# Performance work log

Hardware: AMD Instinct MI355X
Metric: run time of the kernel (lower is better)

The kernel has to match this reference:

```python
import jax, jax.numpy as jnp
import numpy as np

V, H, E = 32000, 1024, 1024
B, S = 64, 128

def setup_inputs() -> dict:
    key = jax.random.key(0)
    ks = jax.random.split(key, 14)
    sc = 0.02
    return {
        "input_batch": jax.random.randint(ks[0], (B, 1), 0, V),
        "prev_h": jax.random.normal(ks[1], (1, B, H), jnp.float32),
        "prev_c": jax.random.normal(ks[2], (1, B, H), jnp.float32),
        "encoder_outputs": jax.random.normal(ks[3], (B, S, H), jnp.float32),
        "lengths": jnp.ones((B,), jnp.int64 if jax.config.read('jax_enable_x64') else jnp.int32),
        "emb": jax.random.normal(ks[4], (V, E), jnp.float32) * sc,
        "attn_w": jax.random.normal(ks[5], (2 * H,), jnp.float32) * sc,
        "attn_b": jax.random.normal(ks[6], (1,), jnp.float32) * sc,
        "W_ih": jax.random.normal(ks[7], (4 * H, E + H), jnp.float32) * sc,
        "W_hh": jax.random.normal(ks[8], (4 * H, H), jnp.float32) * sc,
        "b_ih": jax.random.normal(ks[9], (4 * H,), jnp.float32) * sc,
        "b_hh": jax.random.normal(ks[10], (4 * H,), jnp.float32) * sc,
        "W_out": jax.random.normal(ks[11], (V, H), jnp.float32) * sc,
        "b_out": jax.random.normal(ks[12], (V,), jnp.float32) * sc,
    }

def reference(input_batch, prev_h, prev_c, encoder_outputs, lengths,
              emb, attn_w, attn_b, W_ih, W_hh, b_ih, b_hh, W_out, b_out):
    h0 = prev_h[0]            # [B, H]
    c0 = prev_c[0]            # [B, H]
    x_emb = emb[input_batch[:, 0]]  # [B, E]

    # attention: score[b,s] = concat(h0[b], enc[b,s]) @ attn_w + attn_b
    # (vectorized form of the original per-element Python loop)
    h_part = h0 @ attn_w[:H]                                   # [B]
    e_part = jnp.einsum('bsh,h->bs', encoder_outputs, attn_w[H:])  # [B, S]
    scores = e_part + h_part[:, None] + attn_b[0]
    attn_weights = jax.nn.softmax(scores, axis=-1)             # [B, S]
    context = jnp.einsum('bs,bsh->bh', attn_weights, encoder_outputs)  # [B, H]

    # single-step LSTM cell (torch gate order: i, f, g, o)
    x = jnp.concatenate([x_emb, context], axis=-1)             # [B, E+H]
    gates = x @ W_ih.T + h0 @ W_hh.T + b_ih + b_hh             # [B, 4H]
    i_g, f_g, g_g, o_g = jnp.split(gates, 4, axis=-1)
    c1 = jax.nn.sigmoid(f_g) * c0 + jax.nn.sigmoid(i_g) * jnp.tanh(g_g)
    h1 = jax.nn.sigmoid(o_g) * jnp.tanh(c1)

    # zero-out rows with length == 0
    zmask = (lengths == 0)[:, None]                            # [B, 1]
    h1 = jnp.where(zmask, 0.0, h1)
    c1 = jnp.where(zmask, 0.0, c1)

    logits = h1 @ W_out.T + b_out                              # [B, V]
    logprobs = jax.nn.log_softmax(logits, axis=-1)
    return (logprobs, h1[None], c1[None], attn_weights)
```

## Files before the change

kernel.cpp:

```cpp
#include <hip/hip_runtime.h>
#include <math.h>

constexpr int V = 32000, H = 1024, E = 1024, B = 64, S = 128;
constexpr int KX = 2048;

constexpr long long OUT_H1   = (long long)B * V;
constexpr long long OUT_C1   = OUT_H1 + (long long)B * H;
constexpr long long OUT_ATTN = OUT_C1 + (long long)B * H;

constexpr long long WS_SCORES = 0;
constexpr long long WS_XCAT   = WS_SCORES + (long long)B * S;
constexpr long long WS_PART   = WS_XCAT + (long long)B * KX;
constexpr long long WS_CTXP   = WS_PART + 6LL * B * 4096;
constexpr long long WS_PM     = WS_CTXP + 4LL * B * H;
constexpr long long WS_PL     = WS_PM + 64 * 512;
constexpr long long WS_LC     = WS_PL + 64 * 512;

typedef __attribute__((ext_vector_type(8))) short short8;
typedef __attribute__((ext_vector_type(4))) float f32x4;

__device__ __forceinline__ unsigned short f2bf(float f) {
  unsigned u = __float_as_uint(f);
  u += 0x7FFF + ((u >> 16) & 1);
  return (unsigned short)(u >> 16);
}

__device__ __forceinline__ short8 pack8(float4 a, float4 b) {
  short8 s;
  s[0] = (short)f2bf(a.x); s[1] = (short)f2bf(a.y);
  s[2] = (short)f2bf(a.z); s[3] = (short)f2bf(a.w);
  s[4] = (short)f2bf(b.x); s[5] = (short)f2bf(b.y);
  s[6] = (short)f2bf(b.z); s[7] = (short)f2bf(b.w);
  return s;
}

__device__ __forceinline__ void gemm_body(
    const float* __restrict__ W, int ldw,
    const float* __restrict__ X, int ldx,
    int g0, int k0, int KC,
    float* __restrict__ dst, int ldo, const float* __restrict__ bias,
    float* __restrict__ pm, float* __restrict__ pl) {
  __shared__ __align__(16) unsigned short Wl[64 * 64];
  __shared__ __align__(16) unsigned short Xl[64 * 64];
  __shared__ float pmx[4][64];
  __shared__ float psm[4][64];
  int t = threadIdx.x;
  int lane = t & 63, wid = t >> 6;
  int n = lane & 15, quad = lane >> 4;
  int r0 = t >> 3,          c0 = t & 7;
  int r1 = (t + 256) >> 3,  c1 = (t + 256) & 7;
  int ws0 = r0 * 64 + (c0 ^ (r0 & 7)) * 8;
  int ws1 = r1 * 64 + (c1 ^ (r1 & 7)) * 8;
  f32x4 acc[4] = {{0.f,0.f,0.f,0.f},{0.f,0.f,0.f,0.f},
                  {0.f,0.f,0.f,0.f},{0.f,0.f,0.f,0.f}};
  const float* wp0 = W + (long long)(g0 + r0) * ldw + k0 + c0 * 8;
  const float* wp1 = W + (long long)(g0 + r1) * ldw + k0 + c1 * 8;
  const float* xp0 = X + (long long)r0 * ldx + k0 + c0 * 8;
  const float* xp1 = X + (long long)r1 * ldx + k0 + c1 * 8;
  float4 wa = ((const float4*)wp0)[0], wb = ((const float4*)wp0)[1];
  float4 wc = ((const float4*)wp1)[0], wd = ((const float4*)wp1)[1];
  float4 xa = ((const float4*)xp0)[0], xb = ((const float4*)xp0)[1];
  float4 xc = ((const float4*)xp1)[0], xd = ((const float4*)xp1)[1];

  for (int kt = 0; kt < KC; kt += 64) {
    __syncthreads();
    *(short8*)&Wl[ws0] = pack8(wa, wb);
    *(short8*)&Wl[ws1] = pack8(wc, wd);
    *(short8*)&Xl[ws0] = pack8(xa, xb);
    *(short8*)&Xl[ws1] = pack8(xc, xd);
    __syncthreads();
    if (kt + 64 < KC) {
      int o = kt + 64;
      wa = *(const float4*)(wp0 + o); wb = *(const float4*)(wp0 + o + 4);
      wc = *(const float4*)(wp1 + o); wd = *(const float4*)(wp1 + o + 4);
      xa = *(const float4*)(xp0 + o); xb = *(const float4*)(xp0 + o + 4);
      xc = *(const float4*)(xp1 + o); xd = *(const float4*)(xp1 + o + 4);
    }
#pragma unroll
    for (int kc = 0; kc < 2; ++kc) {
      short8 af = *(const short8*)&Wl[(wid * 16 + n) * 64 +
                                      (((kc * 4 + quad) ^ (n & 7)) * 8)];
#pragma unroll
      for (int nt = 0; nt < 4; ++nt) {
        short8 bf = *(const short8*)&Xl[(nt * 16 + n) * 64 +
                                        (((kc * 4 + quad) ^ (n & 7)) * 8)];
        acc[nt] = __builtin_amdgcn_mfma_f32_16x16x32_bf16(af, bf, acc[nt], 0, 0, 0);
      }
    }
  }
  int gl = wid * 16 + quad * 4;
  float bs[4] = {0.f, 0.f, 0.f, 0.f};
  if (bias) {
#pragma unroll
    for (int r = 0; r < 4; ++r) bs[r] = bias[g0 + gl + r];
  }
  float v[4][4];
#pragma unroll
  for (int nt = 0; nt < 4; ++nt) {
    int b = nt * 16 + n;
#pragma unroll
    for (int r = 0; r < 4; ++r) {
      v[nt][r] = acc[nt][r] + bs[r];
      dst[(long long)b * ldo + g0 + gl + r] = v[nt][r];
    }
  }
  if (pm) {
    float tmax[4];
#pragma unroll
    for (int nt = 0; nt < 4; ++nt) {
      tmax[nt] = fmaxf(fmaxf(v[nt][0], v[nt][1]), fmaxf(v[nt][2], v[nt][3]));
      tmax[nt] = fmaxf(tmax[nt], __shfl_xor(tmax[nt], 16, 64));
      tmax[nt] = fmaxf(tmax[nt], __shfl_xor(tmax[nt], 32, 64));
    }
    if (lane < 16) {
#pragma unroll
      for (int nt = 0; nt < 4; ++nt) pmx[wid][nt * 16 + lane] = tmax[nt];
    }
    __syncthreads();
    float bmax[4], tsum[4];
#pragma unroll
    for (int nt = 0; nt < 4; ++nt) {
      bmax[nt] = fmaxf(fmaxf(pmx[0][nt * 16 + n], pmx[1][nt * 16 + n]),
                       fmaxf(pmx[2][nt * 16 + n], pmx[3][nt * 16 + n]));
      tsum[nt] = __expf(v[nt][0] - bmax[nt]) + __expf(v[nt][1] - bmax[nt]) +
                 __expf(v[nt][2] - bmax[nt]) + __expf(v[nt][3] - bmax[nt]);
      tsum[nt] += __shfl_xor(tsum[nt], 16, 64);
      tsum[nt] += __shfl_xor(tsum[nt], 32, 64);
    }
    if (lane < 16) {
#pragma unroll
      for (int nt = 0; nt < 4; ++nt) psm[wid][nt * 16 + lane] = tsum[nt];
    }
    __syncthreads();
    if (t < 64) {
      float M = fmaxf(fmaxf(pmx[0][t], pmx[1][t]), fmaxf(pmx[2][t], pmx[3][t]));
      float L = psm[0][t] + psm[1][t] + psm[2][t] + psm[3][t];
      pm[t * 512 + blockIdx.x] = M;
      pl[t * 512 + blockIdx.x] = L;
    }
  }
}

__global__ __launch_bounds__(256) void k_gates_mfma(
    const float* __restrict__ W_ih, const float* __restrict__ xcat,
    const float* __restrict__ W_hh, const float* __restrict__ h0,
    float* __restrict__ part) {
  int y = blockIdx.y;
  if (y < 4)
    gemm_body(W_ih, KX, xcat, KX, blockIdx.x * 64, y * 512, 512,
              part + (long long)y * B * 4096, 4096, nullptr, nullptr, nullptr);
  else
    gemm_body(W_hh, H, h0, H, blockIdx.x * 64, (y - 4) * 512, 512,
              part + (long long)y * B * 4096, 4096, nullptr, nullptr, nullptr);
}

__global__ __launch_bounds__(256) void k_logits_mfma(
    const float* __restrict__ W_out, const float* __restrict__ h1,
    float* __restrict__ logits, const float* __restrict__ b_out,
    float* __restrict__ pm, float* __restrict__ pl) {
  gemm_body(W_out, H, h1, H, blockIdx.x * 64, 0, H, logits, V, b_out, pm, pl);
}

__global__ __launch_bounds__(256) void k_scores(
    const float* __restrict__ enc, const float* __restrict__ attn_w,
    float* __restrict__ scores) {
  int w = (blockIdx.x * 256 + threadIdx.x) >> 6;
  int lane = threadIdx.x & 63;
  const float4* e4 = (const float4*)(enc + (long long)w * H);
  const float4* w4 = (const float4*)(attn_w + H);
  float acc = 0.f;
#pragma unroll
  for (int i = 0; i < 4; ++i) {
    float4 a = e4[lane + 64 * i];
    float4 b = w4[lane + 64 * i];
    acc += a.x * b.x + a.y * b.y + a.z * b.z + a.w * b.w;
  }
#pragma unroll
  for (int m = 32; m; m >>= 1) acc += __shfl_xor(acc, m, 64);
  if (lane == 0) scores[w] = acc;
}

__global__ __launch_bounds__(128) void k_softmax(
    const float* __restrict__ scores, const float* __restrict__ h0,
    const float* __restrict__ attn_w, const float* __restrict__ attn_b,
    float* __restrict__ attn_out) {
  __shared__ float red[128];
  int b = blockIdx.x, t = threadIdx.x;
  float p = 0.f;
#pragma unroll
  for (int j = 0; j < 8; ++j) {
    int k = t + 128 * j;
    p += h0[b * H + k] * attn_w[k];
  }
  red[t] = p; __syncthreads();
  for (int off = 64; off > 0; off >>= 1) {
    if (t < off) red[t] += red[t + off];
    __syncthreads();
  }
  float hp = red[0]; __syncthreads();
  float sc = scores[b * S + t] + hp + attn_b[0];
  red[t] = sc; __syncthreads();
  for (int off = 64; off > 0; off >>= 1) {
    if (t < off) red[t] = fmaxf(red[t], red[t + off]);
    __syncthreads();
  }
  float m = red[0]; __syncthreads();
  float e = expf(sc - m);
  red[t] = e; __syncthreads();
  for (int off = 64; off > 0; off >>= 1) {
    if (t < off) red[t] += red[t + off];
    __syncthreads();
  }
  attn_out[b * S + t] = e / red[0];
}

__global__ __launch_bounds__(256) void k_ctx(
    const float* __restrict__ enc, const float* __restrict__ aw_in,
    float* __restrict__ ctxp) {
  __shared__ float aw[32];
  int b = blockIdx.x, sq = blockIdx.y, t = threadIdx.x;
  if (t < 32) aw[t] = aw_in[b * S + sq * 32 + t];
  __syncthreads();
  const float4* e4 = (const float4*)enc;
  float4 acc = {0.f, 0.f, 0.f, 0.f};
  for (int s = 0; s < 32; ++s) {
    float a = aw[s];
    float4 v = e4[(long long)(b * S + sq * 32 + s) * (H / 4) + t];
    acc.x += a * v.x; acc.y += a * v.y; acc.z += a * v.z; acc.w += a * v.w;
  }
  ((float4*)ctxp)[(long long)(sq * B + b) * (H / 4) + t] = acc;
}

__global__ __launch_bounds__(256) void k_xcat(
    const float* __restrict__ ctxp, const float* __restrict__ emb,
    const int* __restrict__ idx, float* __restrict__ xcat) {
  int ft = blockIdx.x * 256 + threadIdx.x;
  int b = ft >> 8, hq = ft & 255;
  const float4* c4 = (const float4*)ctxp;
  float4 ctx = c4[(0 * B + b) * 256 + hq];
#pragma unroll
  for (int sq = 1; sq < 4; ++sq) {
    float4 v = c4[(sq * B + b) * 256 + hq];
    ctx.x += v.x; ctx.y += v.y; ctx.z += v.z; ctx.w += v.w;
  }
  float4* x4 = (float4*)xcat;
  x4[b * 512 + hq]       = ((const float4*)emb)[(long long)idx[b] * 256 + hq];
  x4[b * 512 + 256 + hq] = ctx;
}

__global__ __launch_bounds__(256) void k_lstm(
    const float* __restrict__ part, const float* __restrict__ b_ih,
    const float* __restrict__ b_hh, const float* __restrict__ c0,
    const int* __restrict__ lengths,
    float* __restrict__ h1, float* __restrict__ c1) {
  int ft = blockIdx.x * 256 + threadIdx.x;
  int b = ft >> 10, h = ft & 1023;
  float gs[4] = {0.f, 0.f, 0.f, 0.f};
  for (int ks = 0; ks < 6; ++ks) {
    const float* p = part + (long long)(ks * B + b) * 4096;
#pragma unroll
    for (int q = 0; q < 4; ++q) gs[q] += p[q * H + h];
  }
#pragma unroll
  for (int q = 0; q < 4; ++q) gs[q] += b_ih[q * H + h] + b_hh[q * H + h];
  float ig = 1.f / (1.f + expf(-gs[0]));
  float fg = 1.f / (1.f + expf(-gs[1]));
  float gg = tanhf(gs[2]);
  float og = 1.f / (1.f + expf(-gs[3]));
  float c = fg * c0[ft] + ig * gg;
  float hh = og * tanhf(c);
  if (lengths[b] == 0) { c = 0.f; hh = 0.f; }
  h1[ft] = hh; c1[ft] = c;
}

__global__ __launch_bounds__(256) void k_lsm_comb(
    const float* __restrict__ pm, const float* __restrict__ pl,
    float* __restrict__ lc) {
  __shared__ float red[256];
  int b = blockIdx.x, t = threadIdx.x;
  float v0 = pm[b * 512 + t];
  float v1 = (t + 256 < 500) ? pm[b * 512 + t + 256] : -INFINITY;
  red[t] = fmaxf(v0, v1); __syncthreads();
  for (int off = 128; off; off >>= 1) {
    if (t < off) red[t] = fmaxf(red[t], red[t + off]);
    __syncthreads();
  }
  float M = red[0]; __syncthreads();
  float s = pl[b * 512 + t] * __expf(v0 - M);
  if (t + 256 < 500) s += pl[b * 512 + t + 256] * __expf(v1 - M);
  red[t] = s; __syncthreads();
  for (int off = 128; off; off >>= 1) {
    if (t < off) red[t] += red[t + off];
    __syncthreads();
  }
  if (t == 0) lc[b] = M + logf(red[0]);
}

__global__ __launch_bounds__(256) void k_lsm_fin(
    float* __restrict__ logits, const float* __restrict__ lc) {
  int fi = blockIdx.x * 256 + threadIdx.x;
  float4* p = (float4*)logits;
  float4 x = p[fi];
  float c = lc[fi / 8000];
  x.x -= c; x.y -= c; x.z -= c; x.w -= c;
  p[fi] = x;
}

extern "C" void kernel_launch(void* const* d_in, const int* in_sizes, int n_in,
                              void* d_out, int out_size, void* d_ws, size_t ws_size,
                              hipStream_t stream) {
  const int*   input_batch = (const int*)d_in[0];
  const float* prev_h = (const float*)d_in[1];
  const float* prev_c = (const float*)d_in[2];
  const float* enc    = (const float*)d_in[3];
  const int*   lengths= (const int*)d_in[4];
  const float* emb    = (const float*)d_in[5];
  const float* attn_w = (const float*)d_in[6];
  const float* attn_b = (const float*)d_in[7];
  const float* W_ih   = (const float*)d_in[8];
  const float* W_hh   = (const float*)d_in[9];
  const float* b_ih   = (const float*)d_in[10];
  const float* b_hh   = (const float*)d_in[11];
  const float* W_out  = (const float*)d_in[12];
  const float* b_out  = (const float*)d_in[13];

  float* out = (float*)d_out;
  float* ws  = (float*)d_ws;

  float* scores = ws + WS_SCORES;
  float* xcat   = ws + WS_XCAT;
  float* part   = ws + WS_PART;
  float* ctxp   = ws + WS_CTXP;
  float* pm     = ws + WS_PM;
  float* pl     = ws + WS_PL;
  float* lc     = ws + WS_LC;

  float* logits = out;
  float* h1     = out + OUT_H1;
  float* c1     = out + OUT_C1;
  float* attn   = out + OUT_ATTN;

  k_scores <<<dim3(B * S / 4), 256, 0, stream>>>(enc, attn_w, scores);
  k_softmax<<<dim3(B),         128, 0, stream>>>(scores, prev_h, attn_w, attn_b, attn);
  k_ctx    <<<dim3(B, 4),      256, 0, stream>>>(enc, attn, ctxp);
  k_xcat   <<<dim3(B * H / 1024), 256, 0, stream>>>(ctxp, emb, input_batch, xcat);

  k_gates_mfma<<<dim3(64, 6), 256, 0, stream>>>(W_ih, xcat, W_hh, prev_h, part);
  k_lstm   <<<dim3(B * H / 256), 256, 0, stream>>>(part, b_ih, b_hh, prev_c,
                                                   lengths, h1, c1);

  k_logits_mfma<<<dim3(V / 64), 256, 0, stream>>>(W_out, h1, logits, b_out, pm, pl);

  k_lsm_comb<<<dim3(B), 256, 0, stream>>>(pm, pl, lc);
  k_lsm_fin <<<dim3(B * V / 4 / 256), 256, 0, stream>>>(logits, lc);
}
```

Before: 354.2 us.

## Fuse attention stages into one kernel and logits+log-softmax into cooperative kernel

The scores, softmax, context and xcat kernels are merged into a single per-batch attention kernel, so the scores and context partials no longer round-trip through global memory. The logits GEMM, the log-softmax combine and the finalize pass are merged into one cooperative kernel that separates the phases with grid-wide syncs. This removes several kernel launches and intermediate buffers. In exchange the attention stage runs on only 64 blocks, which may underuse the GPU. The cooperative launch also needs all 500 blocks co-resident, and grid.sync has its own cost.

```diff
diff --git a/kernel.cpp b/kernel.cpp
--- a/kernel.cpp
+++ b/kernel.cpp
@@ -1,5 +1,8 @@
 #include <hip/hip_runtime.h>
+#include <hip/hip_cooperative_groups.h>
 #include <math.h>
+
+namespace cg = cooperative_groups;
 
 constexpr int V = 32000, H = 1024, E = 1024, B = 64, S = 128;
 constexpr int KX = 2048;
@@ -154,98 +157,77 @@
               part + (long long)y * B * 4096, 4096, nullptr, nullptr, nullptr);
 }
 
-__global__ __launch_bounds__(256) void k_logits_mfma(
-    const float* __restrict__ W_out, const float* __restrict__ h1,
-    float* __restrict__ logits, const float* __restrict__ b_out,
-    float* __restrict__ pm, float* __restrict__ pl) {
-  gemm_body(W_out, H, h1, H, blockIdx.x * 64, 0, H, logits, V, b_out, pm, pl);
-}
-
-__global__ __launch_bounds__(256) void k_scores(
-    const float* __restrict__ enc, const float* __restrict__ attn_w,
-    float* __restrict__ scores) {
-  int w = (blockIdx.x * 256 + threadIdx.x) >> 6;
-  int lane = threadIdx.x & 63;
-  const float4* e4 = (const float4*)(enc + (long long)w * H);
-  const float4* w4 = (const float4*)(attn_w + H);
-  float acc = 0.f;
-#pragma unroll
-  for (int i = 0; i < 4; ++i) {
-    float4 a = e4[lane + 64 * i];
-    float4 b = w4[lane + 64 * i];
-    acc += a.x * b.x + a.y * b.y + a.z * b.z + a.w * b.w;
-  }
-#pragma unroll
-  for (int m = 32; m; m >>= 1) acc += __shfl_xor(acc, m, 64);
-  if (lane == 0) scores[w] = acc;
-}
-
-__global__ __launch_bounds__(128) void k_softmax(
-    const float* __restrict__ scores, const float* __restrict__ h0,
+__global__ __launch_bounds__(256) void k_attn(
+    const float* __restrict__ enc, const float* __restrict__ h0,
     const float* __restrict__ attn_w, const float* __restrict__ attn_b,
-    float* __restrict__ attn_out) {
-  __shared__ float red[128];
+    const float* __restrict__ emb, const int* __restrict__ idx,
+    float* __restrict__ attn_out, float* __restrict__ xcat) {
+  __shared__ float red[256];
+  __shared__ float aw[S];
   int b = blockIdx.x, t = threadIdx.x;
-  float p = 0.f;
-#pragma unroll
-  for (int j = 0; j < 8; ++j) {
-    int k = t + 128 * j;
-    p += h0[b * H + k] * attn_w[k];
-  }
-  red[t] = p; __syncthreads();
-  for (int off = 64; off > 0; off >>= 1) {
+  int lane = t & 63, wv = t >> 6;
+  const float4* h4  = (const float4*)(h0 + (long long)b * H);
+  const float4* w4l = (const float4*)attn_w;
+  float4 hv = h4[t], wvv = w4l[t];
+  float p = hv.x * wvv.x + hv.y * wvv.y + hv.z * wvv.z + hv.w * wvv.w;
+#pragma unroll
+  for (int m = 32; m; m >>= 1) p += __shfl_xor(p, m, 64);
+  if (lane == 0) red[wv] = p;
+  __syncthreads();
+  float hp = red[0] + red[1] + red[2] + red[3] + attn_b[0];
+  const float4* w4h = (const float4*)(attn_w + H);
+  float4 wreg[4];
+#pragma unroll
+  for (int j = 0; j < 4; ++j) wreg[j] = w4h[lane + 64 * j];
+  __syncthreads();
+  for (int i = 0; i < 32; ++i) {
+    int s = wv * 32 + i;
+    const float4* e4 = (const float4*)(enc + (long long)(b * S + s) * H);
+    float a = 0.f;
+#pragma unroll
+    for (int j = 0; j < 4; ++j) {
+      float4 e = e4[lane + 64 * j];
+      a += e.x * wreg[j].x + e.y * wreg[j].y + e.z * wreg[j].z + e.w * wreg[j].w;
+    }
+#pragma unroll
+    for (int m = 32; m; m >>= 1) a += __shfl_xor(a, m, 64);
+    if (lane == 0) aw[s] = a + hp;
+  }
+  __syncthreads();
+  float sc = (t < S) ? aw[t] : -INFINITY;
+  red[t] = sc; __syncthreads();
+  for (int off = 128; off; off >>= 1) {
+    if (t < off) red[t] = fmaxf(red[t], red[t + off]);
+    __syncthreads();
+  }
+  float mx = red[0]; __syncthreads();
+  float e = (t < S) ? __expf(sc - mx) : 0.f;
+  red[t] = e; __syncthreads();
+  for (int off = 128; off; off >>= 1) {
     if (t < off) red[t] += red[t + off];
     __syncthreads();
   }
-  float hp = red[0]; __syncthreads();
-  float sc = scores[b * S + t] + hp + attn_b[0];
-  red[t] = sc; __syncthreads();
-  for (int off = 64; off > 0; off >>= 1) {
-    if (t < off) red[t] = fmaxf(red[t], red[t + off]);
-    __syncthreads();
-  }
-  float m = red[0]; __syncthreads();
-  float e = expf(sc - m);
-  red[t] = e; __syncthreads();
-  for (int off = 64; off > 0; off >>= 1) {
-    if (t < off) red[t] += red[t + off];
-    __syncthreads();
-  }
-  attn_out[b * S + t] = e / red[0];
-}
-
-__global__ __launch_bounds__(256) void k_ctx(
-    const float* __restrict__ enc, const float* __restrict__ aw_in,
-    float* __restrict__ ctxp) {
-  __shared__ float aw[32];
-  int b = blockIdx.x, sq = blockIdx.y, t = threadIdx.x;
-  if (t < 32) aw[t] = aw_in[b * S + sq * 32 + t];
+  float inv = 1.f / red[0];
+  if (t < S) {
+    float w = e * inv;
+    aw[t] = w;
+    attn_out[(long long)b * S + t] = w;
+  }
   __syncthreads();
-  const float4* e4 = (const float4*)enc;
-  float4 acc = {0.f, 0.f, 0.f, 0.f};
-  for (int s = 0; s < 32; ++s) {
-    float a = aw[s];
-    float4 v = e4[(long long)(b * S + sq * 32 + s) * (H / 4) + t];
-    acc.x += a * v.x; acc.y += a * v.y; acc.z += a * v.z; acc.w += a * v.w;
-  }
-  ((float4*)ctxp)[(long long)(sq * B + b) * (H / 4) + t] = acc;
-}
-
-__global__ __launch_bounds__(256) void k_xcat(
-    const float* __restrict__ ctxp, const float* __restrict__ emb,
-    const int* __restrict__ idx, float* __restrict__ xcat) {
-  int ft = blockIdx.x * 256 + threadIdx.x;
-  int b = ft >> 8, hq = ft & 255;
-  const float4* c4 = (const float4*)ctxp;
-  float4 ctx = c4[(0 * B + b) * 256 + hq];
-#pragma unroll
-  for (int sq = 1; sq < 4; ++sq) {
-    float4 v = c4[(sq * B + b) * 256 + hq];
-    ctx.x += v.x; ctx.y += v.y; ctx.z += v.z; ctx.w += v.w;
-  }
+  const float4* e4 = (const float4*)(enc + (long long)b * S * H);
+  float4 a0 = {0.f,0.f,0.f,0.f}, a1 = {0.f,0.f,0.f,0.f};
+#pragma unroll 4
+  for (int s = 0; s < S; s += 2) {
+    float4 v0 = e4[(long long)s * (H / 4) + t];
+    float4 v1 = e4[(long long)(s + 1) * (H / 4) + t];
+    float c0 = aw[s], c1 = aw[s + 1];
+    a0.x += c0 * v0.x; a0.y += c0 * v0.y; a0.z += c0 * v0.z; a0.w += c0 * v0.w;
+    a1.x += c1 * v1.x; a1.y += c1 * v1.y; a1.z += c1 * v1.z; a1.w += c1 * v1.w;
+  }
+  a0.x += a1.x; a0.y += a1.y; a0.z += a1.z; a0.w += a1.w;
   float4* x4 = (float4*)xcat;
-  x4[b * 512 + hq]       = ((const float4*)emb)[(long long)idx[b] * 256 + hq];
-  x4[b * 512 + 256 + hq] = ctx;
+  x4[b * 512 + 256 + t] = a0;
+  x4[b * 512 + t] = ((const float4*)emb)[(long long)idx[b] * 256 + t];
 }
 
 __global__ __launch_bounds__(256) void k_lstm(
@@ -273,37 +255,42 @@
   h1[ft] = hh; c1[ft] = c;
 }
 
-__global__ __launch_bounds__(256) void k_lsm_comb(
-    const float* __restrict__ pm, const float* __restrict__ pl,
-    float* __restrict__ lc) {
-  __shared__ float red[256];
-  int b = blockIdx.x, t = threadIdx.x;
-  float v0 = pm[b * 512 + t];
-  float v1 = (t + 256 < 500) ? pm[b * 512 + t + 256] : -INFINITY;
-  red[t] = fmaxf(v0, v1); __syncthreads();
-  for (int off = 128; off; off >>= 1) {
-    if (t < off) red[t] = fmaxf(red[t], red[t + off]);
-    __syncthreads();
-  }
-  float M = red[0]; __syncthreads();
-  float s = pl[b * 512 + t] * __expf(v0 - M);
-  if (t + 256 < 500) s += pl[b * 512 + t + 256] * __expf(v1 - M);
-  red[t] = s; __syncthreads();
-  for (int off = 128; off; off >>= 1) {
-    if (t < off) red[t] += red[t + off];
-    __syncthreads();
-  }
-  if (t == 0) lc[b] = M + logf(red[0]);
-}
-
-__global__ __launch_bounds__(256) void k_lsm_fin(
-    float* __restrict__ logits, const float* __restrict__ lc) {
-  int fi = blockIdx.x * 256 + threadIdx.x;
-  float4* p = (float4*)logits;
-  float4 x = p[fi];
-  float c = lc[fi / 8000];
-  x.x -= c; x.y -= c; x.z -= c; x.w -= c;
-  p[fi] = x;
+__global__ __launch_bounds__(256, 2) void k_logits_coop(
+    const float* __restrict__ W_out, const float* __restrict__ h1,
+    float* __restrict__ logits, const float* __restrict__ b_out,
+    float* __restrict__ pm, float* __restrict__ pl, float* __restrict__ lc) {
+  cg::grid_group grid = cg::this_grid();
+  gemm_body(W_out, H, h1, H, blockIdx.x * 64, 0, H, logits, V, b_out, pm, pl);
+  grid.sync();
+  if (blockIdx.x < B) {
+    __shared__ float red[256];
+    int b = blockIdx.x, t = threadIdx.x;
+    float v0 = pm[b * 512 + t];
+    float v1 = (t + 256 < 500) ? pm[b * 512 + t + 256] : -INFINITY;
+    red[t] = fmaxf(v0, v1); __syncthreads();
+    for (int off = 128; off; off >>= 1) {
+      if (t < off) red[t] = fmaxf(red[t], red[t + off]);
+      __syncthreads();
+    }
+    float M = red[0]; __syncthreads();
+    float s2 = pl[b * 512 + t] * __expf(v0 - M);
+    if (t + 256 < 500) s2 += pl[b * 512 + t + 256] * __expf(v1 - M);
+    red[t] = s2; __syncthreads();
+    for (int off = 128; off; off >>= 1) {
+      if (t < off) red[t] += red[t + off];
+      __syncthreads();
+    }
+    if (t == 0) lc[b] = M + logf(red[0]);
+  }
+  grid.sync();
+  float4* p4 = (float4*)logits;
+  const int nf4 = B * V / 4;
+  for (int fi = blockIdx.x * 256 + threadIdx.x; fi < nf4; fi += 500 * 256) {
+    float4 x = p4[fi];
+    float c = lc[fi / 8000];
+    x.x -= c; x.y -= c; x.z -= c; x.w -= c;
+    p4[fi] = x;
+  }
 }
 
 extern "C" void kernel_launch(void* const* d_in, const int* in_sizes, int n_in,
@@ -327,10 +314,8 @@
   float* out = (float*)d_out;
   float* ws  = (float*)d_ws;
 
-  float* scores = ws + WS_SCORES;
   float* xcat   = ws + WS_XCAT;
   float* part   = ws + WS_PART;
-  float* ctxp   = ws + WS_CTXP;
   float* pm     = ws + WS_PM;
   float* pl     = ws + WS_PL;
   float* lc     = ws + WS_LC;
@@ -340,17 +325,15 @@
   float* c1     = out + OUT_C1;
   float* attn   = out + OUT_ATTN;
 
-  k_scores <<<dim3(B * S / 4), 256, 0, stream>>>(enc, attn_w, scores);
-  k_softmax<<<dim3(B),         128, 0, stream>>>(scores, prev_h, attn_w, attn_b, attn);
-  k_ctx    <<<dim3(B, 4),      256, 0, stream>>>(enc, attn, ctxp);
-  k_xcat   <<<dim3(B * H / 1024), 256, 0, stream>>>(ctxp, emb, input_batch, xcat);
+  k_attn<<<dim3(B), 256, 0, stream>>>(enc, prev_h, attn_w, attn_b,
+                                      emb, input_batch, attn, xcat);
 
   k_gates_mfma<<<dim3(64, 6), 256, 0, stream>>>(W_ih, xcat, W_hh, prev_h, part);
-  k_lstm   <<<dim3(B * H / 256), 256, 0, stream>>>(part, b_ih, b_hh, prev_c,
-                                                   lengths, h1, c1);
-
-  k_logits_mfma<<<dim3(V / 64), 256, 0, stream>>>(W_out, h1, logits, b_out, pm, pl);
-
-  k_lsm_comb<<<dim3(B), 256, 0, stream>>>(pm, pl, lc);
-  k_lsm_fin <<<dim3(B * V / 4 / 256), 256, 0, stream>>>(logits, lc);
-}
+  k_lstm<<<dim3(B * H / 256), 256, 0, stream>>>(part, b_ih, b_hh, prev_c,
+                                                lengths, h1, c1);
+
+  void* args[] = {(void*)&W_out, (void*)&h1, (void*)&logits, (void*)&b_out,
+                  (void*)&pm, (void*)&pl, (void*)&lc};
+  hipLaunchCooperativeKernel((const void*)k_logits_coop, dim3(V / 64),
+                             dim3(256), args, 0, stream);
+}
```

Result: slower. 511.6 us (+44.5%).
